# Optimization experiments

Hardware: AMD Instinct MI355X
Metric: run time of the kernel (lower is better)

The kernel has to match this reference:

```python
import jax, jax.numpy as jnp
import numpy as np

N_NODES = 100000


def gcn_conv(x, W, b, src, dst, n_nodes):
    """PyG GCNConv: add self-loops, symmetric normalization, linear, scatter-add, bias."""
    xw = x @ W  # [N, out]
    loop = jnp.arange(n_nodes, dtype=src.dtype)
    src2 = jnp.concatenate([src, loop])  # sources (x_j gathered from here)
    dst2 = jnp.concatenate([dst, loop])  # targets (aggregation index)
    # degree (incl. self-loops) computed at target nodes, unit edge weights
    deg = jax.ops.segment_sum(jnp.ones_like(dst2, dtype=xw.dtype), dst2, num_segments=n_nodes)
    dinv = jnp.where(deg > 0, jax.lax.rsqrt(deg), 0.0)
    norm = dinv[src2] * dinv[dst2]  # [E+N]
    msg = xw[src2] * norm[:, None]  # [E+N, out]  (memory-bound gather)
    out = jax.ops.segment_sum(msg, dst2, num_segments=n_nodes)  # scatter-add
    return out + b


def setup_inputs() -> dict:
    key = jax.random.key(0)
    k1, k2, k3, k4 = jax.random.split(key, 4)
    F_IN, H, C = 128, 128, 64
    E = 1600000
    x = jax.random.normal(k1, (N_NODES, F_IN), dtype=jnp.float32)
    edge_index = jax.random.randint(k2, (2, E), 0, N_NODES, dtype=jnp.int64)
    # Glorot init like PyG GCNConv
    s1 = float(np.sqrt(6.0 / (F_IN + H)))
    s2 = float(np.sqrt(6.0 / (H + C)))
    W1 = jax.random.uniform(k3, (F_IN, H), jnp.float32, -s1, s1)
    W2 = jax.random.uniform(k4, (H, C), jnp.float32, -s2, s2)
    b1 = jnp.zeros((H,), jnp.float32)
    b2 = jnp.zeros((C,), jnp.float32)
    return {"x": x, "edge_index": edge_index, "W1": W1, "b1": b1, "W2": W2, "b2": b2}


def reference(x, edge_index, W1, b1, W2, b2):
    src, dst = edge_index[0], edge_index[1]
    h = gcn_conv(x, W1, b1, src, dst, N_NODES)
    h = jax.nn.relu(h)  # dropout p=0.0 -> identity
    h = gcn_conv(h, W2, b2, src, dst, N_NODES)
    return jax.nn.log_softmax(h, axis=1)
```

## Files before the change

kernel.cpp:

```cpp
#include <hip/hip_runtime.h>
#include <cmath>


#define THREADS 256
#define BSHIFT 8
#define MAXB 512
#define SLAB_E 8192
#define SLAB_C 9984
#define NB_CAST 96
#define ECHUNK 4096

__device__ __forceinline__ unsigned short f2bf(float f) {
    union { float f; unsigned u; } v; v.f = f;
    unsigned r = v.u + 0x7FFFu + ((v.u >> 16) & 1u);
    return (unsigned short)(r >> 16);
}
__device__ __forceinline__ float bf_lo(unsigned u) {
    union { unsigned u; float f; } v; v.u = u << 16; return v.f;
}
__device__ __forceinline__ float bf_hi(unsigned u) {
    union { unsigned u; float f; } v; v.u = u & 0xFFFF0000u; return v.f;
}

typedef __attribute__((ext_vector_type(8))) short bf16x8;
typedef __attribute__((ext_vector_type(4))) float f32x4;

__global__ __launch_bounds__(256) void k_bscatter(const int* __restrict__ src,
                                                  const int* __restrict__ dst, int E, int B,
                                                  const float* __restrict__ W1,
                                                  const float* __restrict__ W2,
                                                  unsigned short* __restrict__ Wt1,
                                                  unsigned short* __restrict__ Wt2,
                                                  int* __restrict__ bfill,
                                                  unsigned* __restrict__ pairs) {
    const int tid = threadIdx.x;
    if (blockIdx.x < NB_CAST) {
        int idx = blockIdx.x * 256 + tid;
        if (idx < 16384) {
            int n = idx >> 7, k = idx & 127;
            Wt1[idx] = f2bf(W1[k * 128 + n]);
        } else {
            int t = idx - 16384;
            int n = t >> 7, k = t & 127;
            Wt2[t] = f2bf(W2[k * 64 + n]);
        }
        return;
    }
    __shared__ int lc[MAXB];
    __shared__ int lbase[MAXB];
    const int e0 = (blockIdx.x - NB_CAST) * ECHUNK;
    for (int i = tid; i < MAXB; i += 256) lc[i] = 0;
    __syncthreads();
#pragma unroll
    for (int k = 0; k < ECHUNK / 1024; k++) {
        int e = e0 + k * 1024 + tid * 4;
        if (e < E) {
            int4 d4 = *(const int4*)&dst[e];
            atomicAdd(&lc[d4.x >> BSHIFT], 1); atomicAdd(&lc[d4.y >> BSHIFT], 1);
            atomicAdd(&lc[d4.z >> BSHIFT], 1); atomicAdd(&lc[d4.w >> BSHIFT], 1);
        }
    }
    __syncthreads();
    for (int b = tid; b < B; b += 256)
        lbase[b] = lc[b] ? atomicAdd(&bfill[b], lc[b]) : 0;
    __syncthreads();
    for (int i = tid; i < MAXB; i += 256) lc[i] = 0;
    __syncthreads();
#pragma unroll
    for (int k = 0; k < ECHUNK / 1024; k++) {
        int e = e0 + k * 1024 + tid * 4;
        if (e < E) {
            int4 s4 = *(const int4*)&src[e];
            int4 d4 = *(const int4*)&dst[e];
            int b0, r;
            b0 = d4.x >> BSHIFT; r = atomicAdd(&lc[b0], 1);
            pairs[(size_t)b0 * SLAB_E + lbase[b0] + r] = ((unsigned)(d4.x & 255) << 24) | (unsigned)s4.x;
            b0 = d4.y >> BSHIFT; r = atomicAdd(&lc[b0], 1);
            pairs[(size_t)b0 * SLAB_E + lbase[b0] + r] = ((unsigned)(d4.y & 255) << 24) | (unsigned)s4.y;
            b0 = d4.z >> BSHIFT; r = atomicAdd(&lc[b0], 1);
            pairs[(size_t)b0 * SLAB_E + lbase[b0] + r] = ((unsigned)(d4.z & 255) << 24) | (unsigned)s4.z;
            b0 = d4.w >> BSHIFT; r = atomicAdd(&lc[b0], 1);
            pairs[(size_t)b0 * SLAB_E + lbase[b0] + r] = ((unsigned)(d4.w & 255) << 24) | (unsigned)s4.w;
        }
    }
}

__global__ __launch_bounds__(256) void k_bbuild(const unsigned* __restrict__ pairs,
                                                const int* __restrict__ bfill, int N,
                                                int* __restrict__ deg,
                                                float* __restrict__ dinv,
                                                int* __restrict__ rowptr,
                                                unsigned* __restrict__ csr_off) {
    __shared__ int ldeg[256], lex[256], lrank[256];
    const int b = blockIdx.x, tid = threadIdx.x;
    const int node0 = b << BSHIFT;
    const unsigned* pb = pairs + (size_t)b * SLAB_E;
    const int cnt_e = bfill[b];
    const int pbase = b * SLAB_C;
    ldeg[tid] = 0;
    __syncthreads();
    for (int e = tid; e < cnt_e; e += 256)
        atomicAdd(&ldeg[pb[e] >> 24], 1);
    __syncthreads();
    int v = ldeg[tid];
    int pd = (v + 7) & ~7;
    lex[tid] = pd; __syncthreads();
    for (int o = 1; o < 256; o <<= 1) {
        int add = (tid >= o) ? lex[tid - o] : 0;
        __syncthreads();
        lex[tid] += add;
        __syncthreads();
    }
    int pexcl = lex[tid] - pd;
    if (node0 + tid < N) {
        deg[node0 + tid] = v;
        dinv[node0 + tid] = rsqrtf((float)(v + 1));
        rowptr[node0 + tid] = pbase + pexcl;
    }
    __syncthreads();
    lex[tid] = pexcl;
    lrank[tid] = 0;
    __syncthreads();
    for (int e = tid; e < cnt_e; e += 256) {
        unsigned p = pb[e];
        int loc = p >> 24;
        int r = atomicAdd(&lrank[loc], 1);
        csr_off[pbase + lex[loc] + r] = (p & 0xFFFFFFu) << 8;
    }
    for (int p = v; p < pd; p++)
        csr_off[pbase + pexcl + p] = ((unsigned)N) << 8;
}

__global__ __launch_bounds__(256) void k_gemm1(const float* __restrict__ A,
                                               const unsigned short* __restrict__ Wt,
                                               const float* __restrict__ dinv,
                                               unsigned short* __restrict__ Out,
                                               unsigned short* __restrict__ zrow,
                                               int M) {
    constexpr int NC = 128, KP = 136;
    __shared__ __align__(16) short Bs[NC * KP];
    const int tid = threadIdx.x;
    const int row0 = blockIdx.x * 64;

    if (blockIdx.x == 0 && tid < NC) zrow[tid] = 0;

    for (int f = tid; f < NC * 16; f += 256) {
        int n = f >> 4, c = (f & 15) * 8;
        *(uint4*)&Bs[n * KP + c] = *(const uint4*)&Wt[n * 128 + c];
    }

    const int wave = tid >> 6, lane = tid & 63;
    const int m = lane & 15, quad = lane >> 4;
    const int row = row0 + 16 * wave + m;
    const int rowc = row < M ? row : (M - 1);

    bf16x8 afr[4];
#pragma unroll
    for (int k = 0; k < 4; k++) {
        float4 lo = *(const float4*)&A[(size_t)rowc * 128 + quad * 8 + 32 * k];
        float4 hi = *(const float4*)&A[(size_t)rowc * 128 + quad * 8 + 32 * k + 4];
        bf16x8 a;
        a[0] = (short)f2bf(lo.x); a[1] = (short)f2bf(lo.y);
        a[2] = (short)f2bf(lo.z); a[3] = (short)f2bf(lo.w);
        a[4] = (short)f2bf(hi.x); a[5] = (short)f2bf(hi.y);
        a[6] = (short)f2bf(hi.z); a[7] = (short)f2bf(hi.w);
        afr[k] = a;
    }
    __syncthreads();

    constexpr int CT = NC / 16;
    f32x4 acc[CT] = {};
    const short* brow = &Bs[m * KP + quad * 8];
#pragma unroll
    for (int k = 0; k < 4; k++) {
#pragma unroll
        for (int c = 0; c < CT; c++) {
            bf16x8 b = *(const bf16x8*)&brow[(size_t)c * 16 * KP + 32 * k];
            acc[c] = __builtin_amdgcn_mfma_f32_16x16x32_bf16(afr[k], b, acc[c], 0, 0, 0);
        }
    }

    __syncthreads();
    short* Cs = Bs;
    const int rbase = 16 * wave + quad * 4;
    float dv[4];
#pragma unroll
    for (int r = 0; r < 4; r++) {
        int gr = row0 + rbase + r;
        dv[r] = dinv[gr < M ? gr : 0];
    }
#pragma unroll
    for (int c = 0; c < CT; c++)
#pragma unroll
        for (int r = 0; r < 4; r++)
            Cs[(rbase + r) * NC + 16 * c + m] = (short)f2bf(acc[c][r] * dv[r]);
    __syncthreads();
    for (int f = tid; f < 64 * NC / 8; f += 256) {
        int r = f / (NC / 8), c = (f % (NC / 8)) * 8;
        if (row0 + r < M)
            *(uint4*)&Out[(size_t)(row0 + r) * NC + c] = *(const uint4*)&Cs[r * NC + c];
    }
}

__global__ __launch_bounds__(256) void k_agg128g2(const unsigned* __restrict__ csr_off,
                                                  const int* __restrict__ rowptr,
                                                  const int* __restrict__ cnt,
                                                  const float* __restrict__ dinv,
                                                  const unsigned char* __restrict__ xwb,
                                                  const float* __restrict__ bias,
                                                  const unsigned short* __restrict__ Wt2,
                                                  unsigned short* __restrict__ hw2,
                                                  unsigned short* __restrict__ zrow,
                                                  int N) {
    constexpr int KP = 136;
    __shared__ __align__(16) short Bs[64 * KP];
    __shared__ __align__(16) short As[16 * KP];
    const int tid = threadIdx.x;
    const int lane = tid & 63, wave = tid >> 6;
    const int g = lane >> 4, sl = lane & 15;
    const int node0 = blockIdx.x * 16;
    const int i = node0 + wave * 4 + g;
    const bool active = (i < N);
    const int ic = active ? i : 0;

    if (blockIdx.x == 0 && tid < 64) zrow[tid] = 0;

    for (int f = tid; f < 64 * 16; f += 256) {
        int n = f >> 4, c = (f & 15) * 8;
        *(uint4*)&Bs[n * KP + c] = *(const uint4*)&Wt2[n * 128 + c];
    }

    const float di = dinv[ic];
    const int slb = sl * 16;
    uint4 u = *(const uint4*)(xwb + ((size_t)ic << 8) + slb);
    float a0 = bf_lo(u.x), a1 = bf_hi(u.x), a2 = bf_lo(u.y), a3 = bf_hi(u.y);
    float a4 = bf_lo(u.z), a5 = bf_hi(u.z), a6 = bf_lo(u.w), a7 = bf_hi(u.w);
    const int start = rowptr[ic];
    const int pc = active ? ((cnt[ic] + 7) & ~7) : 0;
    unsigned s[8];
#pragma unroll
    for (int k = 0; k < 8; k++) s[k] = csr_off[start + k];
    for (int j = 0; j < pc; j += 8) {
        uint4 uu[8];
#pragma unroll
        for (int k = 0; k < 8; k++) uu[k] = *(const uint4*)(xwb + s[k] + slb);
#pragma unroll
        for (int k = 0; k < 8; k++) s[k] = csr_off[start + j + 8 + k];
#pragma unroll
        for (int k = 0; k < 8; k++) {
            a0 += bf_lo(uu[k].x); a1 += bf_hi(uu[k].x);
            a2 += bf_lo(uu[k].y); a3 += bf_hi(uu[k].y);
            a4 += bf_lo(uu[k].z); a5 += bf_hi(uu[k].z);
            a6 += bf_lo(uu[k].w); a7 += bf_hi(uu[k].w);
        }
    }
    float4 b0 = *(const float4*)&bias[8 * sl];
    float4 b1 = *(const float4*)&bias[8 * sl + 4];
    float r0 = fmaxf(di * a0 + b0.x, 0.f);
    float r1 = fmaxf(di * a1 + b0.y, 0.f);
    float r2 = fmaxf(di * a2 + b0.z, 0.f);
    float r3 = fmaxf(di * a3 + b0.w, 0.f);
    float r4 = fmaxf(di * a4 + b1.x, 0.f);
    float r5 = fmaxf(di * a5 + b1.y, 0.f);
    float r6 = fmaxf(di * a6 + b1.z, 0.f);
    float r7 = fmaxf(di * a7 + b1.w, 0.f);
    uint4 o;
    o.x = (unsigned)f2bf(r0) | ((unsigned)f2bf(r1) << 16);
    o.y = (unsigned)f2bf(r2) | ((unsigned)f2bf(r3) << 16);
    o.z = (unsigned)f2bf(r4) | ((unsigned)f2bf(r5) << 16);
    o.w = (unsigned)f2bf(r6) | ((unsigned)f2bf(r7) << 16);
    *(uint4*)&As[(wave * 4 + g) * KP + 8 * sl] = o;
    __syncthreads();

    const int m = lane & 15, quad = lane >> 4;
    f32x4 acc = {};
    const short* arow = &As[m * KP + quad * 8];
    const short* brow = &Bs[(16 * wave + m) * KP + quad * 8];
#pragma unroll
    for (int k = 0; k < 4; k++) {
        bf16x8 a = *(const bf16x8*)&arow[32 * k];
        bf16x8 b = *(const bf16x8*)&brow[32 * k];
        acc = __builtin_amdgcn_mfma_f32_16x16x32_bf16(a, b, acc, 0, 0, 0);
    }
    __syncthreads();
    short* Cs = As;
    float dv[4];
#pragma unroll
    for (int r = 0; r < 4; r++) {
        int gr = node0 + quad * 4 + r;
        dv[r] = dinv[gr < N ? gr : 0];
    }
#pragma unroll
    for (int r = 0; r < 4; r++)
        Cs[(quad * 4 + r) * 64 + 16 * wave + m] = (short)f2bf(acc[r] * dv[r]);
    __syncthreads();
    for (int f = tid; f < 128; f += 256) {
        int r = f >> 3, c = (f & 7) * 8;
        if (node0 + r < N)
            *(uint4*)&hw2[(size_t)(node0 + r) * 64 + c] = *(const uint4*)&Cs[r * 64 + c];
    }
}

__global__ __launch_bounds__(256) void k_agg64b(const unsigned* __restrict__ csr_off,
                                                const int* __restrict__ rowptr,
                                                const int* __restrict__ cnt,
                                                const float* __restrict__ dinv,
                                                const unsigned char* __restrict__ xwb,
                                                const float* __restrict__ bias,
                                                float* __restrict__ out, int N) {
    const int lane = threadIdx.x & 63;
    const int wid = (blockIdx.x * blockDim.x + threadIdx.x) >> 6;
    const int g = lane >> 3, sl = lane & 7;
    const int i = wid * 8 + g;
    if (i >= N) return;
    const float di = dinv[i];
    const int slb = sl * 16;
    uint4 u = *(const uint4*)(xwb + ((size_t)i << 7) + slb);
    float a0 = bf_lo(u.x), a1 = bf_hi(u.x), a2 = bf_lo(u.y), a3 = bf_hi(u.y);
    float a4 = bf_lo(u.z), a5 = bf_hi(u.z), a6 = bf_lo(u.w), a7 = bf_hi(u.w);
    const int start = rowptr[i];
    const int pc = (cnt[i] + 7) & ~7;
    unsigned s[8];
#pragma unroll
    for (int k = 0; k < 8; k++) s[k] = csr_off[start + k];
    for (int j = 0; j < pc; j += 8) {
        uint4 uu[8];
#pragma unroll
        for (int k = 0; k < 8; k++) uu[k] = *(const uint4*)(xwb + (s[k] >> 1) + slb);
#pragma unroll
        for (int k = 0; k < 8; k++) s[k] = csr_off[start + j + 8 + k];
#pragma unroll
        for (int k = 0; k < 8; k++) {
            a0 += bf_lo(uu[k].x); a1 += bf_hi(uu[k].x);
            a2 += bf_lo(uu[k].y); a3 += bf_hi(uu[k].y);
            a4 += bf_lo(uu[k].z); a5 += bf_hi(uu[k].z);
            a6 += bf_lo(uu[k].w); a7 += bf_hi(uu[k].w);
        }
    }
    float4 b0 = *(const float4*)&bias[8 * sl];
    float4 b1 = *(const float4*)&bias[8 * sl + 4];
    float v0 = di * a0 + b0.x, v1 = di * a1 + b0.y;
    float v2 = di * a2 + b0.z, v3 = di * a3 + b0.w;
    float v4 = di * a4 + b1.x, v5 = di * a5 + b1.y;
    float v6 = di * a6 + b1.z, v7 = di * a7 + b1.w;
    float m = fmaxf(fmaxf(fmaxf(v0, v1), fmaxf(v2, v3)),
                    fmaxf(fmaxf(v4, v5), fmaxf(v6, v7)));
#pragma unroll
    for (int o = 4; o > 0; o >>= 1) m = fmaxf(m, __shfl_xor(m, o));
    float s2 = expf(v0 - m) + expf(v1 - m) + expf(v2 - m) + expf(v3 - m) +
               expf(v4 - m) + expf(v5 - m) + expf(v6 - m) + expf(v7 - m);
#pragma unroll
    for (int o = 4; o > 0; o >>= 1) s2 += __shfl_xor(s2, o);
    float ls = m + logf(s2);
    *(float4*)&out[(size_t)i * 64 + 8 * sl] = make_float4(v0 - ls, v1 - ls, v2 - ls, v3 - ls);
    *(float4*)&out[(size_t)i * 64 + 8 * sl + 4] = make_float4(v4 - ls, v5 - ls, v6 - ls, v7 - ls);
}

extern "C" void kernel_launch(void* const* d_in, const int* in_sizes, int n_in,
                              void* d_out, int out_size, void* d_ws, size_t ws_size,
                              hipStream_t stream) {
    const float* x  = (const float*)d_in[0];
    const int*   ei = (const int*)d_in[1];
    const float* W1 = (const float*)d_in[2];
    const float* b1 = (const float*)d_in[3];
    const float* W2 = (const float*)d_in[4];
    const float* b2 = (const float*)d_in[5];

    const int N = in_sizes[0] / 128;
    const int E = in_sizes[1] / 2;
    const int* src = ei;
    const int* dst = ei + E;
    const int B = (N + 255) >> BSHIFT;
    const int NBLK = (E + ECHUNK - 1) / ECHUNK;

    char* ws = (char*)d_ws;
    size_t off = 0;
    auto alloc = [&](size_t bytes) {
        void* p = ws + off;
        off += (bytes + 255) & ~(size_t)255;
        return p;
    };
    int*            bfill   = (int*)alloc(MAXB * 4);
    int*            deg     = (int*)alloc((size_t)N * 4);
    float*          dinv    = (float*)alloc((size_t)N * 4);
    int*            rowptr  = (int*)alloc((size_t)N * 4);
    unsigned*       csr_off = (unsigned*)alloc(((size_t)B * SLAB_C + 64) * 4);
    unsigned*       pairs   = (unsigned*)alloc((size_t)B * SLAB_E * 4);
    unsigned short* Wt1     = (unsigned short*)alloc(128 * 128 * 2);
    unsigned short* Wt2     = (unsigned short*)alloc(64 * 128 * 2);
    unsigned short* xw1     = (unsigned short*)alloc((size_t)(N + 1) * 128 * 2);
    unsigned short* hw2     = (unsigned short*)alloc((size_t)(N + 1) * 64 * 2);
    float*          outp    = (float*)d_out;

    hipMemsetAsync(bfill, 0, MAXB * 4, stream);

    k_bscatter<<<NB_CAST + NBLK, THREADS, 0, stream>>>(src, dst, E, B, W1, W2, Wt1, Wt2,
                                                       bfill, pairs);
    k_bbuild<<<B, THREADS, 0, stream>>>(pairs, bfill, N, deg, dinv, rowptr, csr_off);

    k_gemm1<<<(N + 63) / 64, THREADS, 0, stream>>>(
        x, Wt1, dinv, xw1, xw1 + (size_t)N * 128, N);
    k_agg128g2<<<(N + 15) / 16, THREADS, 0, stream>>>(
        csr_off, rowptr, deg, dinv, (const unsigned char*)xw1, b1, Wt2,
        hw2, hw2 + (size_t)N * 64, N);
    k_agg64b<<<(N + 31) / 32, THREADS, 0, stream>>>(
        csr_off, rowptr, deg, dinv, (const unsigned char*)hw2, b2, outp, N);
}
```

Measured before the change: 240.2 us.

## Halve scatter chunk, reuse dst loads, widen bucket build to 512 threads, pad store tile

Scatter blocks now cover half as many edges each, so more blocks run, and each thread keeps its dst int4 values in registers between the count pass and the fill pass instead of reloading them. The bucket-build kernel launches 512 threads per bucket so the edge loops stride wider, while the prefix scan stays on the first 256 threads behind guards. The output staging tile in the fused aggregation kernel gets a padded row pitch of 72 to cut LDS bank conflicts. The risks are more per-block global atomics on bfill, idle threads during the scan, and an ECHUNK value that must still match the NBLK computation.

Result: slower. 245.9 us (+2.4%).

```diff
diff --git a/kernel.cpp b/kernel.cpp
--- a/kernel.cpp
+++ b/kernel.cpp
@@ -8,7 +8,8 @@
 #define SLAB_E 8192
 #define SLAB_C 9984
 #define NB_CAST 96
-#define ECHUNK 4096
+#define ECHUNK 2048
+#define CSP 72
 
 __device__ __forceinline__ unsigned short f2bf(float f) {
     union { float f; unsigned u; } v; v.f = f;
@@ -51,13 +52,16 @@
     const int e0 = (blockIdx.x - NB_CAST) * ECHUNK;
     for (int i = tid; i < MAXB; i += 256) lc[i] = 0;
     __syncthreads();
-#pragma unroll
-    for (int k = 0; k < ECHUNK / 1024; k++) {
+    int4 d4[2];
+    bool ok[2];
+#pragma unroll
+    for (int k = 0; k < 2; k++) {
         int e = e0 + k * 1024 + tid * 4;
-        if (e < E) {
-            int4 d4 = *(const int4*)&dst[e];
-            atomicAdd(&lc[d4.x >> BSHIFT], 1); atomicAdd(&lc[d4.y >> BSHIFT], 1);
-            atomicAdd(&lc[d4.z >> BSHIFT], 1); atomicAdd(&lc[d4.w >> BSHIFT], 1);
+        ok[k] = (e < E);
+        if (ok[k]) {
+            d4[k] = *(const int4*)&dst[e];
+            atomicAdd(&lc[d4[k].x >> BSHIFT], 1); atomicAdd(&lc[d4[k].y >> BSHIFT], 1);
+            atomicAdd(&lc[d4[k].z >> BSHIFT], 1); atomicAdd(&lc[d4[k].w >> BSHIFT], 1);
         }
     }
     __syncthreads();
@@ -67,25 +71,24 @@
     for (int i = tid; i < MAXB; i += 256) lc[i] = 0;
     __syncthreads();
 #pragma unroll
-    for (int k = 0; k < ECHUNK / 1024; k++) {
+    for (int k = 0; k < 2; k++) {
         int e = e0 + k * 1024 + tid * 4;
-        if (e < E) {
+        if (ok[k]) {
             int4 s4 = *(const int4*)&src[e];
-            int4 d4 = *(const int4*)&dst[e];
             int b0, r;
-            b0 = d4.x >> BSHIFT; r = atomicAdd(&lc[b0], 1);
-            pairs[(size_t)b0 * SLAB_E + lbase[b0] + r] = ((unsigned)(d4.x & 255) << 24) | (unsigned)s4.x;
-            b0 = d4.y >> BSHIFT; r = atomicAdd(&lc[b0], 1);
-            pairs[(size_t)b0 * SLAB_E + lbase[b0] + r] = ((unsigned)(d4.y & 255) << 24) | (unsigned)s4.y;
-            b0 = d4.z >> BSHIFT; r = atomicAdd(&lc[b0], 1);
-            pairs[(size_t)b0 * SLAB_E + lbase[b0] + r] = ((unsigned)(d4.z & 255) << 24) | (unsigned)s4.z;
-            b0 = d4.w >> BSHIFT; r = atomicAdd(&lc[b0], 1);
-            pairs[(size_t)b0 * SLAB_E + lbase[b0] + r] = ((unsigned)(d4.w & 255) << 24) | (unsigned)s4.w;
-        }
-    }
-}
-
-__global__ __launch_bounds__(256) void k_bbuild(const unsigned* __restrict__ pairs,
+            b0 = d4[k].x >> BSHIFT; r = atomicAdd(&lc[b0], 1);
+            pairs[(size_t)b0 * SLAB_E + lbase[b0] + r] = ((unsigned)(d4[k].x & 255) << 24) | (unsigned)s4.x;
+            b0 = d4[k].y >> BSHIFT; r = atomicAdd(&lc[b0], 1);
+            pairs[(size_t)b0 * SLAB_E + lbase[b0] + r] = ((unsigned)(d4[k].y & 255) << 24) | (unsigned)s4.y;
+            b0 = d4[k].z >> BSHIFT; r = atomicAdd(&lc[b0], 1);
+            pairs[(size_t)b0 * SLAB_E + lbase[b0] + r] = ((unsigned)(d4[k].z & 255) << 24) | (unsigned)s4.z;
+            b0 = d4[k].w >> BSHIFT; r = atomicAdd(&lc[b0], 1);
+            pairs[(size_t)b0 * SLAB_E + lbase[b0] + r] = ((unsigned)(d4[k].w & 255) << 24) | (unsigned)s4.w;
+        }
+    }
+}
+
+__global__ __launch_bounds__(512) void k_bbuild(const unsigned* __restrict__ pairs,
                                                 const int* __restrict__ bfill, int N,
                                                 int* __restrict__ deg,
                                                 float* __restrict__ dinv,
@@ -97,38 +100,48 @@
     const unsigned* pb = pairs + (size_t)b * SLAB_E;
     const int cnt_e = bfill[b];
     const int pbase = b * SLAB_C;
-    ldeg[tid] = 0;
-    __syncthreads();
-    for (int e = tid; e < cnt_e; e += 256)
+    if (tid < 256) ldeg[tid] = 0;
+    __syncthreads();
+    for (int e = tid; e < cnt_e; e += 512)
         atomicAdd(&ldeg[pb[e] >> 24], 1);
     __syncthreads();
-    int v = ldeg[tid];
-    int pd = (v + 7) & ~7;
-    lex[tid] = pd; __syncthreads();
+    int v = 0, pd = 0;
+    if (tid < 256) {
+        v = ldeg[tid];
+        pd = (v + 7) & ~7;
+        lex[tid] = pd;
+    }
+    __syncthreads();
     for (int o = 1; o < 256; o <<= 1) {
-        int add = (tid >= o) ? lex[tid - o] : 0;
+        int add = (tid >= o && tid < 256) ? lex[tid - o] : 0;
         __syncthreads();
-        lex[tid] += add;
+        if (tid < 256) lex[tid] += add;
         __syncthreads();
     }
-    int pexcl = lex[tid] - pd;
-    if (node0 + tid < N) {
-        deg[node0 + tid] = v;
-        dinv[node0 + tid] = rsqrtf((float)(v + 1));
-        rowptr[node0 + tid] = pbase + pexcl;
-    }
-    __syncthreads();
-    lex[tid] = pexcl;
-    lrank[tid] = 0;
-    __syncthreads();
-    for (int e = tid; e < cnt_e; e += 256) {
+    int pexcl = 0;
+    if (tid < 256) {
+        pexcl = lex[tid] - pd;
+        if (node0 + tid < N) {
+            deg[node0 + tid] = v;
+            dinv[node0 + tid] = rsqrtf((float)(v + 1));
+            rowptr[node0 + tid] = pbase + pexcl;
+        }
+    }
+    __syncthreads();
+    if (tid < 256) {
+        lex[tid] = pexcl;
+        lrank[tid] = 0;
+    }
+    __syncthreads();
+    for (int e = tid; e < cnt_e; e += 512) {
         unsigned p = pb[e];
         int loc = p >> 24;
         int r = atomicAdd(&lrank[loc], 1);
         csr_off[pbase + lex[loc] + r] = (p & 0xFFFFFFu) << 8;
     }
-    for (int p = v; p < pd; p++)
-        csr_off[pbase + pexcl + p] = ((unsigned)N) << 8;
+    if (tid < 256)
+        for (int p = v; p < pd; p++)
+            csr_off[pbase + pexcl + p] = ((unsigned)N) << 8;
 }
 
 __global__ __launch_bounds__(256) void k_gemm1(const float* __restrict__ A,
@@ -292,12 +305,12 @@
     }
 #pragma unroll
     for (int r = 0; r < 4; r++)
-        Cs[(quad * 4 + r) * 64 + 16 * wave + m] = (short)f2bf(acc[r] * dv[r]);
+        Cs[(quad * 4 + r) * CSP + 16 * wave + m] = (short)f2bf(acc[r] * dv[r]);
     __syncthreads();
     for (int f = tid; f < 128; f += 256) {
         int r = f >> 3, c = (f & 7) * 8;
         if (node0 + r < N)
-            *(uint4*)&hw2[(size_t)(node0 + r) * 64 + c] = *(const uint4*)&Cs[r * 64 + c];
+            *(uint4*)&hw2[(size_t)(node0 + r) * 64 + c] = *(const uint4*)&Cs[r * CSP + c];
     }
 }
 
@@ -396,7 +409,7 @@
 
     k_bscatter<<<NB_CAST + NBLK, THREADS, 0, stream>>>(src, dst, E, B, W1, W2, Wt1, Wt2,
                                                        bfill, pairs);
-    k_bbuild<<<B, THREADS, 0, stream>>>(pairs, bfill, N, deg, dinv, rowptr, csr_off);
+    k_bbuild<<<B, 512, 0, stream>>>(pairs, bfill, N, deg, dinv, rowptr, csr_off);
 
     k_gemm1<<<(N + 63) / 64, THREADS, 0, stream>>>(
         x, Wt1, dinv, xw1, xw1 + (size_t)N * 128, N);
```
